# Kernel tuning notes

Measured on AMD Instinct MI355X. Metric: run time of the kernel, lower is better.

The kernel has to match this reference:

```python
import jax, jax.numpy as jnp
import numpy as np

EPS = 1e-5
HEADS, DK, DV = 8, 32, 64
SCALE = DK ** -0.5

def _bn(x, gamma, beta, mean, var):
    # eval-mode BatchNorm1d over channel dim of [b, c, n]
    inv = gamma / jnp.sqrt(var + EPS)
    return (x - mean[None, :, None]) * inv[None, :, None] + beta[None, :, None]

def setup_inputs() -> dict:
    key = jax.random.key(0)
    ks = jax.random.split(key, 24)
    dim, n, dim_out = 256, 1024, 256
    idk, idv = DK * HEADS, DV * HEADS
    def bn_params(k, c):
        k1, k2, k3, k4 = jax.random.split(k, 4)
        return (jax.random.normal(k1, (c,)) * 0.1 + 1.0,   # gamma
                jax.random.normal(k2, (c,)) * 0.1,          # beta
                jax.random.normal(k3, (c,)) * 0.1,          # running mean
                jax.random.uniform(k4, (c,)) * 0.5 + 0.5)   # running var > 0
    q_g, q_b, q_m, q_v = bn_params(ks[1], idk)
    k_g, k_b, k_m, k_v = bn_params(ks[2], idk)
    v_g, v_b, v_m, v_v = bn_params(ks[3], idv)
    o_g, o_b, o_m, o_v = bn_params(ks[4], dim_out)
    return {
        'x': jax.random.normal(ks[0], (8, dim, n), dtype=jnp.float32),
        'Wq': jax.random.normal(ks[5], (idk, dim)) * (dim ** -0.5),
        'Wk': jax.random.normal(ks[6], (idk, dim)) * (dim ** -0.5),
        'Wv': jax.random.normal(ks[7], (idv, dim)) * (dim ** -0.5),
        'Wo': jax.random.normal(ks[8], (dim_out, idv)) * (idv ** -0.5),
        'bo': jax.random.normal(ks[9], (dim_out,)) * 0.02,
        'pos_emb': jax.random.normal(ks[10], (n, HEADS)) * 0.02,
        'q_gamma': q_g, 'q_beta': q_b, 'q_mean': q_m, 'q_var': q_v,
        'k_gamma': k_g, 'k_beta': k_b, 'k_mean': k_m, 'k_var': k_v,
        'v_gamma': v_g, 'v_beta': v_b, 'v_mean': v_m, 'v_var': v_v,
        'o_gamma': o_g, 'o_beta': o_b, 'o_mean': o_m, 'o_var': o_v,
    }

def reference(x, Wq, Wk, Wv, Wo, bo, pos_emb,
              q_gamma, q_beta, q_mean, q_var,
              k_gamma, k_beta, k_mean, k_var,
              v_gamma, v_beta, v_mean, v_var,
              o_gamma, o_beta, o_mean, o_var):
    b, _, n = x.shape
    # 1x1 conv == channel matmul, then BN
    q = _bn(jnp.einsum('bcn,oc->bon', x, Wq), q_gamma, q_beta, q_mean, q_var)
    k = _bn(jnp.einsum('bcn,oc->bon', x, Wk), k_gamma, k_beta, k_mean, k_var)
    v = _bn(jnp.einsum('bcn,oc->bon', x, Wv), v_gamma, v_beta, v_mean, v_var)
    # b (h d) n -> b h n d
    q = q.reshape(b, HEADS, DK, n).transpose(0, 1, 3, 2)
    k = k.reshape(b, HEADS, DK, n).transpose(0, 1, 3, 2)
    v = v.reshape(b, HEADS, DV, n).transpose(0, 1, 3, 2)
    dots = jnp.einsum('bhid,bhjd->bhij', q, k) * SCALE
    # relative-position bias: emb[|i-j|] -> [n, n, h] -> [1, h, n, n]
    rel = jnp.abs(jnp.arange(n)[:, None] - jnp.arange(n)[None, :])
    bias = pos_emb[rel].transpose(2, 0, 1)[None]
    dots = dots + bias / SCALE
    attn = jax.nn.softmax(dots, axis=-1)
    out = jnp.einsum('bhij,bhjd->bhid', attn, v)
    # b h n d -> b (h d) n
    out = out.transpose(0, 1, 3, 2).reshape(b, HEADS * DV, n)
    out = jax.nn.gelu(out, approximate=False)
    out = jnp.einsum('bcn,oc->bon', out, Wo) + bo[None, :, None]
    return _bn(out, o_gamma, o_beta, o_mean, o_var)
```

## Files before the change

### kernel.cpp

```cpp
#include <hip/hip_runtime.h>
#include <hip/hip_bf16.h>

#define HEADS 8
#define DK 32
#define DV 64
#define DIM 256
#define NCTX 1024
#define NB 8
#define IDK 256
#define IDV 512
#define SCALE 0.17677669529663687f
#define INV_SCALE 5.656854249492381f
#define LOG2E 1.4426950408889634f
#define BN_EPS 1e-5f
#define THR 11.5416f

typedef __bf16 bf16x8 __attribute__((ext_vector_type(8)));
typedef __bf16 bf16x4 __attribute__((ext_vector_type(4)));
typedef float f32x4 __attribute__((ext_vector_type(4)));
typedef float f32x16 __attribute__((ext_vector_type(16)));

static __device__ __forceinline__ unsigned short bfbits(float v) {
  __bf16 b = (__bf16)v;
  return __builtin_bit_cast(unsigned short, b);
}

__global__ __launch_bounds__(256) void k_prep_trans(
    const float* __restrict__ x,
    const float* __restrict__ Wq, const float* __restrict__ Wk,
    const float* __restrict__ Wv, const float* __restrict__ Wo,
    const float* __restrict__ bo, const float* __restrict__ pe,
    const float* __restrict__ qg, const float* __restrict__ qb,
    const float* __restrict__ qm, const float* __restrict__ qv,
    const float* __restrict__ kg, const float* __restrict__ kb,
    const float* __restrict__ km, const float* __restrict__ kv,
    const float* __restrict__ vg, const float* __restrict__ vb,
    const float* __restrict__ vm, const float* __restrict__ vv,
    const float* __restrict__ og, const float* __restrict__ ob,
    const float* __restrict__ om, const float* __restrict__ ov,
    __bf16* __restrict__ xT, __bf16* __restrict__ WB, float* __restrict__ BB,
    uint2* __restrict__ Tq4g) {
  int bid = blockIdx.x;
  if (bid < 1605) {
    int idx = bid * 256 + threadIdx.x;
    if (idx < 65536) {
      int o = idx >> 8;
      WB[idx] = (__bf16)(Wq[idx] * (qg[o] * rsqrtf(qv[o] + BN_EPS) * SCALE * LOG2E));
    } else if (idx < 131072) {
      int i = idx - 65536, o = i >> 8;
      WB[idx] = (__bf16)(Wk[i] * (kg[o] * rsqrtf(kv[o] + BN_EPS)));
    } else if (idx < 262144) {
      int i = idx - 131072, o = i >> 8;
      WB[idx] = (__bf16)(Wv[i] * (vg[o] * rsqrtf(vv[o] + BN_EPS)));
    } else if (idx < 393216) {
      int i = idx - 262144, o = i >> 9;
      WB[idx] = (__bf16)(Wo[i] * (og[o] * rsqrtf(ov[o] + BN_EPS)));
    } else if (idx < 394496) {
      int i = idx - 393216;
      if (i < 256) {
        float sc = qg[i] * rsqrtf(qv[i] + BN_EPS);
        BB[i] = (qb[i] - qm[i] * sc) * SCALE * LOG2E;
      } else if (i < 512) {
        int o = i - 256;
        float sc = kg[o] * rsqrtf(kv[o] + BN_EPS);
        BB[i] = kb[o] - km[o] * sc;
      } else if (i < 1024) {
        int o = i - 512;
        float sc = vg[o] * rsqrtf(vv[o] + BN_EPS);
        BB[i] = vb[o] - vm[o] * sc;
      } else {
        int o = i - 1024;
        float sc = og[o] * rsqrtf(ov[o] + BN_EPS);
        BB[i] = (bo[o] - om[o]) * sc + ob[o];
      }
    } else {
      int i = idx - 394496;
      int h = i >> 11, t = i & 2047;
      unsigned short us[4];
#pragma unroll
      for (int rr = 0; rr < 4; ++rr) {
        int d = t - rr - 1023; d = d < 0 ? -d : d; d = d > 1023 ? 1023 : d;
        us[rr] = bfbits(pe[(size_t)d * HEADS + h] * INV_SCALE * LOG2E);
      }
      uint2 e;
      e.x = (unsigned)us[0] | ((unsigned)us[1] << 16);
      e.y = (unsigned)us[2] | ((unsigned)us[3] << 16);
      Tq4g[((size_t)h << 11) + t] = e;
    }
  } else {
    __shared__ float t[64][65];
    int tb = bid - 1605;
    int b = tb >> 6, c0 = ((tb >> 4) & 3) * 64, n0 = (tb & 15) * 64;
    int col = threadIdx.x & 63, rb = threadIdx.x >> 6;
    const float* xp = x + ((size_t)b * DIM + c0) * NCTX + n0;
#pragma unroll
    for (int r = 0; r < 16; ++r) {
      int row = rb + 4 * r;
      t[row][col] = xp[(size_t)row * NCTX + col];
    }
    __syncthreads();
    __bf16* op = xT + ((size_t)b * NCTX + n0) * DIM + c0;
#pragma unroll
    for (int r = 0; r < 16; ++r) {
      int i = rb + 4 * r;
      op[(size_t)i * DIM + col] = (__bf16)t[col][i];
    }
  }
}

__global__ __launch_bounds__(256, 2) void k_gemm_qkv(
    const __bf16* __restrict__ Xsrc, const __bf16* __restrict__ Wsrc,
    const float* __restrict__ Bias, __bf16* __restrict__ Qws,
    __bf16* __restrict__ Kws, __bf16* __restrict__ Vws) {
  int bx = blockIdx.x, by = blockIdx.y;
  int mode = by < 2 ? 0 : (by < 4 ? 1 : 2);
  int tid = threadIdx.x, wave = tid >> 6, lane = tid & 63;
  int wm = wave >> 1, wn = wave & 1;
  int l16 = lane & 15, g = (lane >> 4) & 3, g4 = g * 4;
  int R0 = bx * 128;

  __shared__ __align__(16) char XTl[16384];
  __shared__ __align__(16) char WTl[16384];

  int sr = tid >> 1, sh = tid & 1;
  const __bf16* xg = Xsrc + (size_t)(R0 + sr) * DIM + sh * 32;
  const __bf16* wg = Wsrc + (size_t)(by * 128 + sr) * DIM + sh * 32;
  int wbase = sr * 128;
  int gsw[4];
#pragma unroll
  for (int q = 0; q < 4; ++q) gsw[q] = ((sh * 4 + q) ^ (sr & 7)) * 16;

  bf16x8 sx[4], sw[4];
#pragma unroll
  for (int q = 0; q < 4; ++q) {
    sx[q] = *reinterpret_cast<const bf16x8*>(xg + q * 8);
    sw[q] = *reinterpret_cast<const bf16x8*>(wg + q * 8);
  }

  f32x4 acc[4][4] = {};
  const char* Abase = (mode <= 1) ? WTl : XTl;
  const char* Bbase = (mode <= 1) ? XTl : WTl;

  for (int st = 0; st < 4; ++st) {
    __syncthreads();
#pragma unroll
    for (int q = 0; q < 4; ++q) {
      *reinterpret_cast<bf16x8*>(XTl + wbase + gsw[q]) = sx[q];
      *reinterpret_cast<bf16x8*>(WTl + wbase + gsw[q]) = sw[q];
    }
    __syncthreads();
    if (st + 1 < 4) {
      const __bf16* xn = xg + (st + 1) * 64;
      const __bf16* wn_ = wg + (st + 1) * 64;
#pragma unroll
      for (int q = 0; q < 4; ++q) {
        sx[q] = *reinterpret_cast<const bf16x8*>(xn + q * 8);
        sw[q] = *reinterpret_cast<const bf16x8*>(wn_ + q * 8);
      }
    }
#pragma unroll
    for (int kc = 0; kc < 2; ++kc) {
      bf16x8 af[4], bf[4];
#pragma unroll
      for (int t = 0; t < 4; ++t) {
        int ra = wm * 64 + t * 16 + l16;
        af[t] = *reinterpret_cast<const bf16x8*>(
            Abase + ra * 128 + (((kc * 4 + g) ^ (ra & 7)) * 16));
        int rb = wn * 64 + t * 16 + l16;
        bf[t] = *reinterpret_cast<const bf16x8*>(
            Bbase + rb * 128 + (((kc * 4 + g) ^ (rb & 7)) * 16));
      }
      __builtin_amdgcn_s_setprio(1);
#pragma unroll
      for (int mt = 0; mt < 4; ++mt)
#pragma unroll
        for (int nt = 0; nt < 4; ++nt)
          acc[mt][nt] = __builtin_amdgcn_mfma_f32_16x16x32_bf16(
              af[mt], bf[nt], acc[mt][nt], 0, 0, 0);
      __builtin_amdgcn_s_setprio(0);
    }
  }

  if (mode <= 1) {
    __bf16* OWS = (mode == 0) ? Qws : Kws;
    const float* bb = Bias + (mode == 0 ? 0 : 256);
    int oq0 = by * 128 - (mode == 1 ? 256 : 0) + wm * 64;
#pragma unroll
    for (int mt = 0; mt < 4; ++mt) {
      int oq = oq0 + mt * 16 + g4;
      float4 b4 = *reinterpret_cast<const float4*>(&bb[oq]);
      int h = oq >> 5, d0 = oq & 31;
#pragma unroll
      for (int nt = 0; nt < 4; ++nt) {
        int i = R0 + wn * 64 + nt * 16 + l16;
        int b = i >> 10, n = i & 1023;
        bf16x4 pk;
        pk[0] = (__bf16)(acc[mt][nt][0] + b4.x);
        pk[1] = (__bf16)(acc[mt][nt][1] + b4.y);
        pk[2] = (__bf16)(acc[mt][nt][2] + b4.z);
        pk[3] = (__bf16)(acc[mt][nt][3] + b4.w);
        *reinterpret_cast<bf16x4*>(
            &OWS[(((size_t)b * HEADS + h) * NCTX + n) * DK + d0]) = pk;
      }
    }
  } else {
#pragma unroll
    for (int nt = 0; nt < 4; ++nt) {
      int vo = (by - 4) * 128 + wn * 64 + nt * 16 + l16;
      float bia = Bias[512 + vo];
#pragma unroll
      for (int mt = 0; mt < 4; ++mt) {
        int i0 = R0 + wm * 64 + mt * 16 + g4;
        int b = i0 >> 10, n = i0 & 1023;
        bf16x4 pk;
#pragma unroll
        for (int rr = 0; rr < 4; ++rr) pk[rr] = (__bf16)(acc[mt][nt][rr] + bia);
        *reinterpret_cast<bf16x4*>(&Vws[((size_t)b * IDV + vo) * NCTX + n]) = pk;
      }
    }
  }
}

__global__ __launch_bounds__(256, 2) void k_gemm_out(
    const __bf16* __restrict__ G, const __bf16* __restrict__ WoB,
    const float* __restrict__ bo2, float* __restrict__ out) {
  int bx = blockIdx.x, by = blockIdx.y;
  int tid = threadIdx.x, wave = tid >> 6, lane = tid & 63;
  int wm = wave >> 1, wn = wave & 1;
  int l16 = lane & 15, g = (lane >> 4) & 3, g4 = g * 4;
  int R0 = bx * 128;

  __shared__ __align__(16) char XTl[16384];
  __shared__ __align__(16) char WTl[8192];

  int sr = tid >> 1, sh = tid & 1;
  const __bf16* xg = G + (size_t)(R0 + sr) * IDV + sh * 32;
  int xbase = sr * 128;
  int gsw[4];
#pragma unroll
  for (int q = 0; q < 4; ++q) gsw[q] = ((sh * 4 + q) ^ (sr & 7)) * 16;

  int wsr = tid >> 2, wq = tid & 3;
  const __bf16* wg = WoB + (size_t)(by * 64 + wsr) * IDV + wq * 16;
  int wbase = wsr * 128;
  int gswW[2];
#pragma unroll
  for (int q = 0; q < 2; ++q) gswW[q] = ((wq * 2 + q) ^ (wsr & 7)) * 16;

  bf16x8 sx[4], sw[2];
#pragma unroll
  for (int q = 0; q < 4; ++q) sx[q] = *reinterpret_cast<const bf16x8*>(xg + q * 8);
#pragma unroll
  for (int q = 0; q < 2; ++q) sw[q] = *reinterpret_cast<const bf16x8*>(wg + q * 8);

  f32x4 acc[4][2] = {};

  for (int st = 0; st < 8; ++st) {
    __syncthreads();
#pragma unroll
    for (int q = 0; q < 4; ++q) *reinterpret_cast<bf16x8*>(XTl + xbase + gsw[q]) = sx[q];
#pragma unroll
    for (int q = 0; q < 2; ++q) *reinterpret_cast<bf16x8*>(WTl + wbase + gswW[q]) = sw[q];
    __syncthreads();
    if (st + 1 < 8) {
      const __bf16* xn = xg + (st + 1) * 64;
      const __bf16* wn_ = wg + (st + 1) * 64;
#pragma unroll
      for (int q = 0; q < 4; ++q) sx[q] = *reinterpret_cast<const bf16x8*>(xn + q * 8);
#pragma unroll
      for (int q = 0; q < 2; ++q) sw[q] = *reinterpret_cast<const bf16x8*>(wn_ + q * 8);
    }
#pragma unroll
    for (int kc = 0; kc < 2; ++kc) {
      bf16x8 af[4], bf[2];
#pragma unroll
      for (int t = 0; t < 4; ++t) {
        int ra = wm * 64 + t * 16 + l16;
        af[t] = *reinterpret_cast<const bf16x8*>(
            XTl + ra * 128 + (((kc * 4 + g) ^ (ra & 7)) * 16));
      }
#pragma unroll
      for (int t = 0; t < 2; ++t) {
        int rb = wn * 32 + t * 16 + l16;
        bf[t] = *reinterpret_cast<const bf16x8*>(
            WTl + rb * 128 + (((kc * 4 + g) ^ (rb & 7)) * 16));
      }
      __builtin_amdgcn_s_setprio(1);
#pragma unroll
      for (int mt = 0; mt < 4; ++mt)
#pragma unroll
        for (int nt = 0; nt < 2; ++nt)
          acc[mt][nt] = __builtin_amdgcn_mfma_f32_16x16x32_bf16(
              af[mt], bf[nt], acc[mt][nt], 0, 0, 0);
      __builtin_amdgcn_s_setprio(0);
    }
  }
#pragma unroll
  for (int nt = 0; nt < 2; ++nt) {
    int o = by * 64 + wn * 32 + nt * 16 + l16;
    float bia = bo2[o];
#pragma unroll
    for (int mt = 0; mt < 4; ++mt) {
      int i0 = R0 + wm * 64 + mt * 16 + g4;
      int b = i0 >> 10, n = i0 & 1023;
      float4 st;
      st.x = acc[mt][nt][0] + bia;
      st.y = acc[mt][nt][1] + bia;
      st.z = acc[mt][nt][2] + bia;
      st.w = acc[mt][nt][3] + bia;
      *reinterpret_cast<float4*>(&out[((size_t)b * DIM + o) * NCTX + n]) = st;
    }
  }
}

__global__ __launch_bounds__(128, 2) void k_attn(
    const __bf16* __restrict__ Qws, const __bf16* __restrict__ Kws,
    const __bf16* __restrict__ Vws, const uint2* __restrict__ Tq4g,
    __bf16* __restrict__ G) {
  int flat = blockIdx.x;
  int swz = (flat & 7) * 128 + (flat >> 3);
  int iblk = swz & 15, bh = swz >> 4;
  int b = bh >> 3, h = bh & 7;
  int tid = threadIdx.x, wave = tid >> 6, lane = tid & 63;
  int l31 = lane & 31, hi = lane >> 5;

  __shared__ __align__(16) __bf16 Vlds[2][64 * 64];
  __shared__ __align__(16) uint2 TqL[1088];

  int i0b = iblk * 64;
  {
    const uint4* tg4 = reinterpret_cast<const uint4*>(Tq4g + ((size_t)h << 11) + i0b);
    uint4* tl4 = reinterpret_cast<uint4*>(TqL);
    for (int c = tid; c < 544; c += 128) tl4[c] = tg4[c];
  }

  int i0w = i0b + wave * 32;
  int irow = i0w + l31;
  const __bf16* qbase = Qws + (size_t)bh * NCTX * DK;
  const __bf16* kbase = Kws + (size_t)bh * NCTX * DK;
  const __bf16* vbase = Vws + ((size_t)b * IDV + h * DV) * NCTX;
  bf16x8 qf0 = *reinterpret_cast<const bf16x8*>(qbase + (size_t)irow * DK + 8 * hi);
  bf16x8 qf1 = *reinterpret_cast<const bf16x8*>(qbase + (size_t)irow * DK + 16 + 8 * hi);

  const __bf16* kp = kbase + (size_t)l31 * DK + 8 * hi;
  bf16x8 ck0 = *reinterpret_cast<const bf16x8*>(kp);
  bf16x8 ck1 = *reinterpret_cast<const bf16x8*>(kp + 16);
  bf16x8 ck2 = *reinterpret_cast<const bf16x8*>(kp + 32 * DK);
  bf16x8 ck3 = *reinterpret_cast<const bf16x8*>(kp + 32 * DK + 16);

  int r_ = tid >> 1, vh = tid & 1;
  const __bf16* vgp = vbase + (size_t)r_ * NCTX + 8 * (vh * 4);
  int vwo[4];
#pragma unroll
  for (int q = 0; q < 4; ++q) vwo[q] = r_ * 64 + 8 * ((vh * 4 + q) ^ (r_ & 7));

  bf16x8 rv[4];
#pragma unroll
  for (int q = 0; q < 4; ++q) rv[q] = *reinterpret_cast<const bf16x8*>(vgp + q * 8);
#pragma unroll
  for (int q = 0; q < 4; ++q) *reinterpret_cast<bf16x8*>(&Vlds[0][0] + vwo[q]) = rv[q];

  f32x16 acc0 = {}, acc1 = {};
  float m = -1e30f, s = 0.0f;
  int kxb = wave * 32 + l31 + 1023 - 4 * hi;
  const bf16x4* Tqp = reinterpret_cast<const bf16x4*>(TqL);

  __syncthreads();

  for (int it = 0; it < 16; ++it) {
    int cur = it & 1, nxt = cur ^ 1;
    int j0 = it * 64;
    int jn = (j0 + 64) & (NCTX - 1);
    bf16x8 nk0 = *reinterpret_cast<const bf16x8*>(kp + (size_t)jn * DK);
    bf16x8 nk1 = *reinterpret_cast<const bf16x8*>(kp + (size_t)jn * DK + 16);
    bf16x8 nk2 = *reinterpret_cast<const bf16x8*>(kp + (size_t)(jn + 32) * DK);
    bf16x8 nk3 = *reinterpret_cast<const bf16x8*>(kp + (size_t)(jn + 32) * DK + 16);
#pragma unroll
    for (int q = 0; q < 4; ++q) rv[q] = *reinterpret_cast<const bf16x8*>(vgp + jn + q * 8);

    float sv[32];
#pragma unroll
    for (int jg = 0; jg < 2; ++jg) {
      f32x16 S = {};
      __builtin_amdgcn_s_setprio(1);
      S = __builtin_amdgcn_mfma_f32_32x32x16_bf16(jg ? ck2 : ck0, qf0, S, 0, 0, 0);
      S = __builtin_amdgcn_mfma_f32_32x32x16_bf16(jg ? ck3 : ck1, qf1, S, 0, 0, 0);
      __builtin_amdgcn_s_setprio(0);
      int kb_ = kxb - j0 - 32 * jg;
#pragma unroll
      for (int q = 0; q < 4; ++q) {
        bf16x4 q4 = Tqp[kb_ - 8 * q];
#pragma unroll
        for (int rr = 0; rr < 4; ++rr)
          sv[jg * 16 + q * 4 + rr] = S[q * 4 + rr] + (float)q4[rr];
      }
    }
    float pmax = sv[0];
#pragma unroll
    for (int k = 1; k < 32; ++k) pmax = fmaxf(pmax, sv[k]);
    if (__any(pmax > m + THR)) {
      float mx = fmaxf(pmax, __shfl_xor(pmax, 32));
      float mnew = fmaxf(m, mx);
      float corr = __builtin_amdgcn_exp2f(m - mnew);
      s *= corr; m = mnew;
#pragma unroll
      for (int r = 0; r < 16; ++r) {
        float cv = __shfl(corr, (r & 3) + 8 * (r >> 2) + 4 * hi);
        acc0[r] *= cv; acc1[r] *= cv;
      }
    }
#pragma unroll
    for (int k = 0; k < 32; ++k) sv[k] = __builtin_amdgcn_exp2f(sv[k] - m);
    float ps = 0.0f;
#pragma unroll
    for (int k = 0; k < 32; ++k) ps += sv[k];
    s += ps;
#pragma unroll
    for (int jg = 0; jg < 2; ++jg) {
#pragma unroll
      for (int u = 0; u < 2; ++u) {
        int base = jg * 16 + 8 * u;
        unsigned we0, we1, wo0, wo1;
        asm("v_cvt_pk_bf16_f32 %0, %1, %2" : "=v"(we0) : "v"(sv[base + 0]), "v"(sv[base + 1]));
        asm("v_cvt_pk_bf16_f32 %0, %1, %2" : "=v"(we1) : "v"(sv[base + 2]), "v"(sv[base + 3]));
        asm("v_cvt_pk_bf16_f32 %0, %1, %2" : "=v"(wo0) : "v"(sv[base + 4]), "v"(sv[base + 5]));
        asm("v_cvt_pk_bf16_f32 %0, %1, %2" : "=v"(wo1) : "v"(sv[base + 6]), "v"(sv[base + 7]));
        asm volatile("v_permlane32_swap_b32 %0, %1" : "+v"(we0), "+v"(wo0));
        asm volatile("v_permlane32_swap_b32 %0, %1" : "+v"(we1), "+v"(wo1));
        uint4 pw = {we0, we1, wo0, wo1};
        bf16x8 pfrag = *reinterpret_cast<bf16x8*>(&pw);
        int sl = 2 * (jg * 2 + u) + hi;
        bf16x8 vf0 = *reinterpret_cast<const bf16x8*>(
            &Vlds[cur][0] + l31 * 64 + 8 * (sl ^ (l31 & 7)));
        bf16x8 vf1 = *reinterpret_cast<const bf16x8*>(
            &Vlds[cur][0] + (32 + l31) * 64 + 8 * (sl ^ (l31 & 7)));
        __builtin_amdgcn_s_setprio(1);
        acc0 = __builtin_amdgcn_mfma_f32_32x32x16_bf16(pfrag, vf0, acc0, 0, 0, 0);
        acc1 = __builtin_amdgcn_mfma_f32_32x32x16_bf16(pfrag, vf1, acc1, 0, 0, 0);
        __builtin_amdgcn_s_setprio(0);
      }
    }
    ck0 = nk0; ck1 = nk1; ck2 = nk2; ck3 = nk3;
#pragma unroll
    for (int q = 0; q < 4; ++q) *reinterpret_cast<bf16x8*>(&Vlds[nxt][0] + vwo[q]) = rv[q];
    __syncthreads();
  }
  float srow = s + __shfl_xor(s, 32);
  float inv = 1.0f / srow;
  __bf16* gbase = G + (size_t)b * NCTX * IDV + h * DV + l31;
#pragma unroll
  for (int r = 0; r < 16; ++r) {
    int il = (r & 3) + 8 * (r >> 2) + 4 * hi;
    float iv = __shfl(inv, il);
    float v0 = acc0[r] * iv, v1 = acc1[r] * iv;
    float g0 = 0.5f * v0 * (1.0f + erff(v0 * 0.70710678118654752f));
    float g1 = 0.5f * v1 * (1.0f + erff(v1 * 0.70710678118654752f));
    gbase[(size_t)(i0w + il) * IDV] = (__bf16)g0;
    gbase[(size_t)(i0w + il) * IDV + 32] = (__bf16)g1;
  }
}

extern "C" void kernel_launch(void* const* d_in, const int* in_sizes, int n_in,
                              void* d_out, int out_size, void* d_ws, size_t ws_size,
                              hipStream_t stream) {
  const float* x  = (const float*)d_in[0];
  const float* Wq = (const float*)d_in[1];
  const float* Wk = (const float*)d_in[2];
  const float* Wv = (const float*)d_in[3];
  const float* Wo = (const float*)d_in[4];
  const float* bo = (const float*)d_in[5];
  const float* pe = (const float*)d_in[6];
  const float* qg = (const float*)d_in[7];
  const float* qb = (const float*)d_in[8];
  const float* qm = (const float*)d_in[9];
  const float* qv = (const float*)d_in[10];
  const float* kg = (const float*)d_in[11];
  const float* kb = (const float*)d_in[12];
  const float* km = (const float*)d_in[13];
  const float* kv = (const float*)d_in[14];
  const float* vg = (const float*)d_in[15];
  const float* vb = (const float*)d_in[16];
  const float* vm = (const float*)d_in[17];
  const float* vv = (const float*)d_in[18];
  const float* og = (const float*)d_in[19];
  const float* ob = (const float*)d_in[20];
  const float* om = (const float*)d_in[21];
  const float* ov = (const float*)d_in[22];

  char* ws = (char*)d_ws;
  __bf16* xT = (__bf16*)(ws);
  __bf16* Q  = (__bf16*)(ws + (4ull << 20));
  __bf16* K  = (__bf16*)(ws + (8ull << 20));
  __bf16* V  = (__bf16*)(ws + (12ull << 20));
  __bf16* G  = (__bf16*)(ws + (20ull << 20));
  __bf16* WB = (__bf16*)(ws + (28ull << 20));
  float*  BB = (float*)(ws + (28ull << 20) + (768ull << 10));
  uint2*  Tq = (uint2*)(ws + (29ull << 20));
  float* out = (float*)d_out;

  k_prep_trans<<<dim3(2117), 256, 0, stream>>>(
      x, Wq, Wk, Wv, Wo, bo, pe, qg, qb, qm, qv, kg, kb, km, kv,
      vg, vb, vm, vv, og, ob, om, ov, xT, WB, BB, Tq);
  k_gemm_qkv<<<dim3(64, 8), 256, 0, stream>>>(xT, WB, BB, Q, K, V);
  k_attn<<<dim3(1024), 128, 0, stream>>>(Q, K, V, Tq, G);
  k_gemm_out<<<dim3(64, 4), 256, 0, stream>>>(G, WB + 262144, BB + 1024, out);
}
```

Baseline: 59.48 us.

## Split attention over key halves with a separate combine kernel

```diff
diff --git a/kernel.cpp b/kernel.cpp
--- a/kernel.cpp
+++ b/kernel.cpp
@@ -313,27 +313,24 @@
   }
 }
 
-__global__ __launch_bounds__(128, 2) void k_attn(
+__global__ __launch_bounds__(128, 3) void k_attn(
     const __bf16* __restrict__ Qws, const __bf16* __restrict__ Kws,
     const __bf16* __restrict__ Vws, const uint2* __restrict__ Tq4g,
-    __bf16* __restrict__ G) {
+    __bf16* __restrict__ Opart, float* __restrict__ MS) {
   int flat = blockIdx.x;
-  int swz = (flat & 7) * 128 + (flat >> 3);
+  int jh = flat >> 10;
+  int rest = flat & 1023;
+  int swz = (rest & 7) * 128 + (rest >> 3);
   int iblk = swz & 15, bh = swz >> 4;
   int b = bh >> 3, h = bh & 7;
   int tid = threadIdx.x, wave = tid >> 6, lane = tid & 63;
   int l31 = lane & 31, hi = lane >> 5;
-
+  int jbase = jh * 512;
+
+  __shared__ __align__(16) __bf16 Klds[2][64][40];
   __shared__ __align__(16) __bf16 Vlds[2][64 * 64];
-  __shared__ __align__(16) uint2 TqL[1088];
 
   int i0b = iblk * 64;
-  {
-    const uint4* tg4 = reinterpret_cast<const uint4*>(Tq4g + ((size_t)h << 11) + i0b);
-    uint4* tl4 = reinterpret_cast<uint4*>(TqL);
-    for (int c = tid; c < 544; c += 128) tl4[c] = tg4[c];
-  }
-
   int i0w = i0b + wave * 32;
   int irow = i0w + l31;
   const __bf16* qbase = Qws + (size_t)bh * NCTX * DK;
@@ -342,54 +339,55 @@
   bf16x8 qf0 = *reinterpret_cast<const bf16x8*>(qbase + (size_t)irow * DK + 8 * hi);
   bf16x8 qf1 = *reinterpret_cast<const bf16x8*>(qbase + (size_t)irow * DK + 16 + 8 * hi);
 
-  const __bf16* kp = kbase + (size_t)l31 * DK + 8 * hi;
-  bf16x8 ck0 = *reinterpret_cast<const bf16x8*>(kp);
-  bf16x8 ck1 = *reinterpret_cast<const bf16x8*>(kp + 16);
-  bf16x8 ck2 = *reinterpret_cast<const bf16x8*>(kp + 32 * DK);
-  bf16x8 ck3 = *reinterpret_cast<const bf16x8*>(kp + 32 * DK + 16);
-
+  int rk_ = tid >> 1, sk2 = tid & 1;
+  const __bf16* kgp = kbase + (size_t)(jbase + rk_) * DK + 16 * sk2;
+  int ko0 = rk_ * 40 + 16 * sk2, ko1 = ko0 + 8;
   int r_ = tid >> 1, vh = tid & 1;
-  const __bf16* vgp = vbase + (size_t)r_ * NCTX + 8 * (vh * 4);
+  const __bf16* vgp = vbase + (size_t)r_ * NCTX + jbase + 8 * (vh * 4);
   int vwo[4];
 #pragma unroll
   for (int q = 0; q < 4; ++q) vwo[q] = r_ * 64 + 8 * ((vh * 4 + q) ^ (r_ & 7));
 
+  bf16x8 rk0 = *reinterpret_cast<const bf16x8*>(kgp);
+  bf16x8 rk1 = *reinterpret_cast<const bf16x8*>(kgp + 8);
   bf16x8 rv[4];
 #pragma unroll
   for (int q = 0; q < 4; ++q) rv[q] = *reinterpret_cast<const bf16x8*>(vgp + q * 8);
+  *reinterpret_cast<bf16x8*>(&Klds[0][0][0] + ko0) = rk0;
+  *reinterpret_cast<bf16x8*>(&Klds[0][0][0] + ko1) = rk1;
 #pragma unroll
   for (int q = 0; q < 4; ++q) *reinterpret_cast<bf16x8*>(&Vlds[0][0] + vwo[q]) = rv[q];
 
   f32x16 acc0 = {}, acc1 = {};
   float m = -1e30f, s = 0.0f;
-  int kxb = wave * 32 + l31 + 1023 - 4 * hi;
-  const bf16x4* Tqp = reinterpret_cast<const bf16x4*>(TqL);
+  int kxg = irow + 1023 - 4 * hi;
+  const bf16x4* TqG = reinterpret_cast<const bf16x4*>(Tq4g + ((size_t)h << 11));
 
   __syncthreads();
 
-  for (int it = 0; it < 16; ++it) {
+  for (int it = 0; it < 8; ++it) {
     int cur = it & 1, nxt = cur ^ 1;
-    int j0 = it * 64;
-    int jn = (j0 + 64) & (NCTX - 1);
-    bf16x8 nk0 = *reinterpret_cast<const bf16x8*>(kp + (size_t)jn * DK);
-    bf16x8 nk1 = *reinterpret_cast<const bf16x8*>(kp + (size_t)jn * DK + 16);
-    bf16x8 nk2 = *reinterpret_cast<const bf16x8*>(kp + (size_t)(jn + 32) * DK);
-    bf16x8 nk3 = *reinterpret_cast<const bf16x8*>(kp + (size_t)(jn + 32) * DK + 16);
+    int j0 = jbase + it * 64;
+    int jn = ((it + 1) & 7) * 64;
+    rk0 = *reinterpret_cast<const bf16x8*>(kgp + (size_t)jn * DK);
+    rk1 = *reinterpret_cast<const bf16x8*>(kgp + (size_t)jn * DK + 8);
 #pragma unroll
     for (int q = 0; q < 4; ++q) rv[q] = *reinterpret_cast<const bf16x8*>(vgp + jn + q * 8);
 
     float sv[32];
 #pragma unroll
     for (int jg = 0; jg < 2; ++jg) {
+      bf16x8 kf0 = *reinterpret_cast<const bf16x8*>(&Klds[cur][32 * jg + l31][8 * hi]);
+      bf16x8 kf1 = *reinterpret_cast<const bf16x8*>(&Klds[cur][32 * jg + l31][16 + 8 * hi]);
       f32x16 S = {};
       __builtin_amdgcn_s_setprio(1);
-      S = __builtin_amdgcn_mfma_f32_32x32x16_bf16(jg ? ck2 : ck0, qf0, S, 0, 0, 0);
-      S = __builtin_amdgcn_mfma_f32_32x32x16_bf16(jg ? ck3 : ck1, qf1, S, 0, 0, 0);
+      S = __builtin_amdgcn_mfma_f32_32x32x16_bf16(kf0, qf0, S, 0, 0, 0);
+      S = __builtin_amdgcn_mfma_f32_32x32x16_bf16(kf1, qf1, S, 0, 0, 0);
       __builtin_amdgcn_s_setprio(0);
-      int kb_ = kxb - j0 - 32 * jg;
+      int kb_ = kxg - j0 - 32 * jg;
 #pragma unroll
       for (int q = 0; q < 4; ++q) {
-        bf16x4 q4 = Tqp[kb_ - 8 * q];
+        bf16x4 q4 = TqG[kb_ - 8 * q];
 #pragma unroll
         for (int rr = 0; rr < 4; ++rr)
           sv[jg * 16 + q * 4 + rr] = S[q * 4 + rr] + (float)q4[rr];
@@ -440,23 +438,59 @@
         __builtin_amdgcn_s_setprio(0);
       }
     }
-    ck0 = nk0; ck1 = nk1; ck2 = nk2; ck3 = nk3;
+    *reinterpret_cast<bf16x8*>(&Klds[nxt][0][0] + ko0) = rk0;
+    *reinterpret_cast<bf16x8*>(&Klds[nxt][0][0] + ko1) = rk1;
 #pragma unroll
     for (int q = 0; q < 4; ++q) *reinterpret_cast<bf16x8*>(&Vlds[nxt][0] + vwo[q]) = rv[q];
     __syncthreads();
   }
   float srow = s + __shfl_xor(s, 32);
-  float inv = 1.0f / srow;
-  __bf16* gbase = G + (size_t)b * NCTX * IDV + h * DV + l31;
+  int blk = bh * 16 + iblk;
+  __bf16* Op = Opart + ((size_t)(jh * 1024 + blk)) * 4096;
+  float* MSp = MS + ((size_t)(jh * 1024 + blk)) * 128;
+  if (hi == 0) {
+    MSp[wave * 32 + l31] = m;
+    MSp[64 + wave * 32 + l31] = srow;
+  }
 #pragma unroll
   for (int r = 0; r < 16; ++r) {
-    int il = (r & 3) + 8 * (r >> 2) + 4 * hi;
-    float iv = __shfl(inv, il);
-    float v0 = acc0[r] * iv, v1 = acc1[r] * iv;
-    float g0 = 0.5f * v0 * (1.0f + erff(v0 * 0.70710678118654752f));
-    float g1 = 0.5f * v1 * (1.0f + erff(v1 * 0.70710678118654752f));
-    gbase[(size_t)(i0w + il) * IDV] = (__bf16)g0;
-    gbase[(size_t)(i0w + il) * IDV + 32] = (__bf16)g1;
+    int row = wave * 32 + (r & 3) + 8 * (r >> 2) + 4 * hi;
+    Op[row * 64 + l31] = (__bf16)acc0[r];
+    Op[row * 64 + 32 + l31] = (__bf16)acc1[r];
+  }
+}
+
+__global__ __launch_bounds__(128) void k_comb(
+    const __bf16* __restrict__ Opart, const float* __restrict__ MS,
+    __bf16* __restrict__ G) {
+  int blk = blockIdx.x;
+  int bh = blk >> 4, iblk = blk & 15;
+  int b = bh >> 3, h = bh & 7;
+  int tid = threadIdx.x;
+  int row = tid >> 1, dh = tid & 1;
+  const __bf16* O1 = Opart + (size_t)blk * 4096 + row * 64 + dh * 32;
+  const __bf16* O2 = Opart + (size_t)(1024 + blk) * 4096 + row * 64 + dh * 32;
+  const float* M1 = MS + (size_t)blk * 128;
+  const float* M2 = MS + (size_t)(1024 + blk) * 128;
+  float m1 = M1[row], s1 = M1[64 + row];
+  float m2 = M2[row], s2 = M2[64 + row];
+  float M = fmaxf(m1, m2);
+  float w1 = __builtin_amdgcn_exp2f(m1 - M);
+  float w2 = __builtin_amdgcn_exp2f(m2 - M);
+  float inv = 1.0f / (s1 * w1 + s2 * w2);
+  w1 *= inv; w2 *= inv;
+  __bf16* gp = G + (size_t)b * NCTX * IDV + (size_t)(iblk * 64 + row) * IDV + h * DV + dh * 32;
+#pragma unroll
+  for (int q = 0; q < 4; ++q) {
+    bf16x8 o1 = *reinterpret_cast<const bf16x8*>(O1 + q * 8);
+    bf16x8 o2 = *reinterpret_cast<const bf16x8*>(O2 + q * 8);
+    bf16x8 rg;
+#pragma unroll
+    for (int j = 0; j < 8; ++j) {
+      float v = (float)o1[j] * w1 + (float)o2[j] * w2;
+      rg[j] = (__bf16)(0.5f * v * (1.0f + erff(v * 0.70710678118654752f)));
+    }
+    *reinterpret_cast<bf16x8*>(gp + q * 8) = rg;
   }
 }
 
@@ -496,12 +530,15 @@
   __bf16* WB = (__bf16*)(ws + (28ull << 20));
   float*  BB = (float*)(ws + (28ull << 20) + (768ull << 10));
   uint2*  Tq = (uint2*)(ws + (29ull << 20));
+  __bf16* Op = (__bf16*)(ws + (32ull << 20));
+  float*  MSb = (float*)(ws + (52ull << 20));
   float* out = (float*)d_out;
 
   k_prep_trans<<<dim3(2117), 256, 0, stream>>>(
       x, Wq, Wk, Wv, Wo, bo, pe, qg, qb, qm, qv, kg, kb, km, kv,
       vg, vb, vm, vv, og, ob, om, ov, xT, WB, BB, Tq);
   k_gemm_qkv<<<dim3(64, 8), 256, 0, stream>>>(xT, WB, BB, Q, K, V);
-  k_attn<<<dim3(1024), 128, 0, stream>>>(Q, K, V, Tq, G);
+  k_attn<<<dim3(2048), 128, 0, stream>>>(Q, K, V, Tq, Op, MSb);
+  k_comb<<<dim3(1024), 128, 0, stream>>>(Op, MSb, G);
   k_gemm_out<<<dim3(64, 4), 256, 0, stream>>>(G, WB + 262144, BB + 1024, out);
 }
```

Result: slower. 74.59 us (+25.4%).

## Process two query tiles per wave and stage K through shared memory

Applied to the files above, without the earlier changes.

```diff
diff --git a/kernel.cpp b/kernel.cpp
--- a/kernel.cpp
+++ b/kernel.cpp
@@ -318,51 +318,54 @@
     const __bf16* __restrict__ Vws, const uint2* __restrict__ Tq4g,
     __bf16* __restrict__ G) {
   int flat = blockIdx.x;
-  int swz = (flat & 7) * 128 + (flat >> 3);
-  int iblk = swz & 15, bh = swz >> 4;
+  int swz = (flat & 7) * 64 + (flat >> 3);
+  int iblk = swz & 7, bh = swz >> 3;
   int b = bh >> 3, h = bh & 7;
   int tid = threadIdx.x, wave = tid >> 6, lane = tid & 63;
   int l31 = lane & 31, hi = lane >> 5;
 
+  __shared__ __align__(16) __bf16 Klds[2][64][40];
   __shared__ __align__(16) __bf16 Vlds[2][64 * 64];
-  __shared__ __align__(16) uint2 TqL[1088];
-
-  int i0b = iblk * 64;
+  __shared__ __align__(16) uint2 TqL[1152];
+
+  int i0b = iblk * 128;
   {
     const uint4* tg4 = reinterpret_cast<const uint4*>(Tq4g + ((size_t)h << 11) + i0b);
     uint4* tl4 = reinterpret_cast<uint4*>(TqL);
-    for (int c = tid; c < 544; c += 128) tl4[c] = tg4[c];
-  }
-
-  int i0w = i0b + wave * 32;
-  int irow = i0w + l31;
+    for (int c = tid; c < 576; c += 128) tl4[c] = tg4[c];
+  }
+
+  int i0w = i0b + wave * 64;
   const __bf16* qbase = Qws + (size_t)bh * NCTX * DK;
   const __bf16* kbase = Kws + (size_t)bh * NCTX * DK;
   const __bf16* vbase = Vws + ((size_t)b * IDV + h * DV) * NCTX;
-  bf16x8 qf0 = *reinterpret_cast<const bf16x8*>(qbase + (size_t)irow * DK + 8 * hi);
-  bf16x8 qf1 = *reinterpret_cast<const bf16x8*>(qbase + (size_t)irow * DK + 16 + 8 * hi);
-
-  const __bf16* kp = kbase + (size_t)l31 * DK + 8 * hi;
-  bf16x8 ck0 = *reinterpret_cast<const bf16x8*>(kp);
-  bf16x8 ck1 = *reinterpret_cast<const bf16x8*>(kp + 16);
-  bf16x8 ck2 = *reinterpret_cast<const bf16x8*>(kp + 32 * DK);
-  bf16x8 ck3 = *reinterpret_cast<const bf16x8*>(kp + 32 * DK + 16);
-
-  int r_ = tid >> 1, vh = tid & 1;
-  const __bf16* vgp = vbase + (size_t)r_ * NCTX + 8 * (vh * 4);
+  bf16x8 qf00 = *reinterpret_cast<const bf16x8*>(qbase + (size_t)(i0w + l31) * DK + 8 * hi);
+  bf16x8 qf01 = *reinterpret_cast<const bf16x8*>(qbase + (size_t)(i0w + l31) * DK + 16 + 8 * hi);
+  bf16x8 qf10 = *reinterpret_cast<const bf16x8*>(qbase + (size_t)(i0w + 32 + l31) * DK + 8 * hi);
+  bf16x8 qf11 = *reinterpret_cast<const bf16x8*>(qbase + (size_t)(i0w + 32 + l31) * DK + 16 + 8 * hi);
+
+  int r_ = tid >> 1, half = tid & 1;
+  const __bf16* kgp = kbase + (size_t)r_ * DK + 16 * half;
+  int ko0 = r_ * 40 + 16 * half, ko1 = ko0 + 8;
+  const __bf16* vgp = vbase + (size_t)r_ * NCTX + 8 * (half * 4);
   int vwo[4];
 #pragma unroll
-  for (int q = 0; q < 4; ++q) vwo[q] = r_ * 64 + 8 * ((vh * 4 + q) ^ (r_ & 7));
-
+  for (int q = 0; q < 4; ++q) vwo[q] = r_ * 64 + 8 * ((half * 4 + q) ^ (r_ & 7));
+
+  bf16x8 rk0 = *reinterpret_cast<const bf16x8*>(kgp);
+  bf16x8 rk1 = *reinterpret_cast<const bf16x8*>(kgp + 8);
   bf16x8 rv[4];
 #pragma unroll
   for (int q = 0; q < 4; ++q) rv[q] = *reinterpret_cast<const bf16x8*>(vgp + q * 8);
+  *reinterpret_cast<bf16x8*>(&Klds[0][0][0] + ko0) = rk0;
+  *reinterpret_cast<bf16x8*>(&Klds[0][0][0] + ko1) = rk1;
 #pragma unroll
   for (int q = 0; q < 4; ++q) *reinterpret_cast<bf16x8*>(&Vlds[0][0] + vwo[q]) = rv[q];
 
-  f32x16 acc0 = {}, acc1 = {};
-  float m = -1e30f, s = 0.0f;
-  int kxb = wave * 32 + l31 + 1023 - 4 * hi;
+  f32x16 acc00 = {}, acc01 = {}, acc10 = {}, acc11 = {};
+  float m0 = -1e30f, s0 = 0.0f, m1 = -1e30f, s1 = 0.0f;
+  int kxb0 = wave * 64 + l31 + 1023 - 4 * hi;
+  int kxb1 = kxb0 + 32;
   const bf16x4* Tqp = reinterpret_cast<const bf16x4*>(TqL);
 
   __syncthreads();
@@ -371,92 +374,149 @@
     int cur = it & 1, nxt = cur ^ 1;
     int j0 = it * 64;
     int jn = (j0 + 64) & (NCTX - 1);
-    bf16x8 nk0 = *reinterpret_cast<const bf16x8*>(kp + (size_t)jn * DK);
-    bf16x8 nk1 = *reinterpret_cast<const bf16x8*>(kp + (size_t)jn * DK + 16);
-    bf16x8 nk2 = *reinterpret_cast<const bf16x8*>(kp + (size_t)(jn + 32) * DK);
-    bf16x8 nk3 = *reinterpret_cast<const bf16x8*>(kp + (size_t)(jn + 32) * DK + 16);
+    rk0 = *reinterpret_cast<const bf16x8*>(kgp + (size_t)jn * DK);
+    rk1 = *reinterpret_cast<const bf16x8*>(kgp + (size_t)jn * DK + 8);
 #pragma unroll
     for (int q = 0; q < 4; ++q) rv[q] = *reinterpret_cast<const bf16x8*>(vgp + jn + q * 8);
 
-    float sv[32];
+    float sv0[32], sv1[32];
 #pragma unroll
     for (int jg = 0; jg < 2; ++jg) {
-      f32x16 S = {};
+      bf16x8 kf0 = *reinterpret_cast<const bf16x8*>(&Klds[cur][32 * jg + l31][8 * hi]);
+      bf16x8 kf1 = *reinterpret_cast<const bf16x8*>(&Klds[cur][32 * jg + l31][16 + 8 * hi]);
+      f32x16 S0 = {}, S1 = {};
       __builtin_amdgcn_s_setprio(1);
-      S = __builtin_amdgcn_mfma_f32_32x32x16_bf16(jg ? ck2 : ck0, qf0, S, 0, 0, 0);
-      S = __builtin_amdgcn_mfma_f32_32x32x16_bf16(jg ? ck3 : ck1, qf1, S, 0, 0, 0);
+      S0 = __builtin_amdgcn_mfma_f32_32x32x16_bf16(kf0, qf00, S0, 0, 0, 0);
+      S1 = __builtin_amdgcn_mfma_f32_32x32x16_bf16(kf0, qf10, S1, 0, 0, 0);
+      S0 = __builtin_amdgcn_mfma_f32_32x32x16_bf16(kf1, qf01, S0, 0, 0, 0);
+      S1 = __builtin_amdgcn_mfma_f32_32x32x16_bf16(kf1, qf11, S1, 0, 0, 0);
       __builtin_amdgcn_s_setprio(0);
-      int kb_ = kxb - j0 - 32 * jg;
+      int kb0 = kxb0 - j0 - 32 * jg;
+      int kb1 = kxb1 - j0 - 32 * jg;
 #pragma unroll
       for (int q = 0; q < 4; ++q) {
-        bf16x4 q4 = Tqp[kb_ - 8 * q];
-#pragma unroll
-        for (int rr = 0; rr < 4; ++rr)
-          sv[jg * 16 + q * 4 + rr] = S[q * 4 + rr] + (float)q4[rr];
-      }
-    }
-    float pmax = sv[0];
-#pragma unroll
-    for (int k = 1; k < 32; ++k) pmax = fmaxf(pmax, sv[k]);
-    if (__any(pmax > m + THR)) {
-      float mx = fmaxf(pmax, __shfl_xor(pmax, 32));
-      float mnew = fmaxf(m, mx);
-      float corr = __builtin_amdgcn_exp2f(m - mnew);
-      s *= corr; m = mnew;
-#pragma unroll
-      for (int r = 0; r < 16; ++r) {
-        float cv = __shfl(corr, (r & 3) + 8 * (r >> 2) + 4 * hi);
-        acc0[r] *= cv; acc1[r] *= cv;
-      }
-    }
-#pragma unroll
-    for (int k = 0; k < 32; ++k) sv[k] = __builtin_amdgcn_exp2f(sv[k] - m);
-    float ps = 0.0f;
-#pragma unroll
-    for (int k = 0; k < 32; ++k) ps += sv[k];
-    s += ps;
+        bf16x4 q40 = Tqp[kb0 - 8 * q];
+        bf16x4 q41 = Tqp[kb1 - 8 * q];
+#pragma unroll
+        for (int rr = 0; rr < 4; ++rr) {
+          sv0[jg * 16 + q * 4 + rr] = S0[q * 4 + rr] + (float)q40[rr];
+          sv1[jg * 16 + q * 4 + rr] = S1[q * 4 + rr] + (float)q41[rr];
+        }
+      }
+    }
+    {
+      float pmax = sv0[0];
+#pragma unroll
+      for (int k = 1; k < 32; ++k) pmax = fmaxf(pmax, sv0[k]);
+      if (__any(pmax > m0 + THR)) {
+        float mx = fmaxf(pmax, __shfl_xor(pmax, 32));
+        float mnew = fmaxf(m0, mx);
+        float corr = __builtin_amdgcn_exp2f(m0 - mnew);
+        s0 *= corr; m0 = mnew;
+#pragma unroll
+        for (int r = 0; r < 16; ++r) {
+          float cv = __shfl(corr, (r & 3) + 8 * (r >> 2) + 4 * hi);
+          acc00[r] *= cv; acc01[r] *= cv;
+        }
+      }
+#pragma unroll
+      for (int k = 0; k < 32; ++k) sv0[k] = __builtin_amdgcn_exp2f(sv0[k] - m0);
+      float ps = 0.0f;
+#pragma unroll
+      for (int k = 0; k < 32; ++k) ps += sv0[k];
+      s0 += ps;
+    }
+    {
+      float pmax = sv1[0];
+#pragma unroll
+      for (int k = 1; k < 32; ++k) pmax = fmaxf(pmax, sv1[k]);
+      if (__any(pmax > m1 + THR)) {
+        float mx = fmaxf(pmax, __shfl_xor(pmax, 32));
+        float mnew = fmaxf(m1, mx);
+        float corr = __builtin_amdgcn_exp2f(m1 - mnew);
+        s1 *= corr; m1 = mnew;
+#pragma unroll
+        for (int r = 0; r < 16; ++r) {
+          float cv = __shfl(corr, (r & 3) + 8 * (r >> 2) + 4 * hi);
+          acc10[r] *= cv; acc11[r] *= cv;
+        }
+      }
+#pragma unroll
+      for (int k = 0; k < 32; ++k) sv1[k] = __builtin_amdgcn_exp2f(sv1[k] - m1);
+      float ps = 0.0f;
+#pragma unroll
+      for (int k = 0; k < 32; ++k) ps += sv1[k];
+      s1 += ps;
+    }
 #pragma unroll
     for (int jg = 0; jg < 2; ++jg) {
 #pragma unroll
       for (int u = 0; u < 2; ++u) {
         int base = jg * 16 + 8 * u;
-        unsigned we0, we1, wo0, wo1;
-        asm("v_cvt_pk_bf16_f32 %0, %1, %2" : "=v"(we0) : "v"(sv[base + 0]), "v"(sv[base + 1]));
-        asm("v_cvt_pk_bf16_f32 %0, %1, %2" : "=v"(we1) : "v"(sv[base + 2]), "v"(sv[base + 3]));
-        asm("v_cvt_pk_bf16_f32 %0, %1, %2" : "=v"(wo0) : "v"(sv[base + 4]), "v"(sv[base + 5]));
-        asm("v_cvt_pk_bf16_f32 %0, %1, %2" : "=v"(wo1) : "v"(sv[base + 6]), "v"(sv[base + 7]));
-        asm volatile("v_permlane32_swap_b32 %0, %1" : "+v"(we0), "+v"(wo0));
-        asm volatile("v_permlane32_swap_b32 %0, %1" : "+v"(we1), "+v"(wo1));
-        uint4 pw = {we0, we1, wo0, wo1};
-        bf16x8 pfrag = *reinterpret_cast<bf16x8*>(&pw);
+        unsigned a0, a1, b0, b1, c0, c1, d0, d1;
+        asm("v_cvt_pk_bf16_f32 %0, %1, %2" : "=v"(a0) : "v"(sv0[base + 0]), "v"(sv0[base + 1]));
+        asm("v_cvt_pk_bf16_f32 %0, %1, %2" : "=v"(a1) : "v"(sv0[base + 2]), "v"(sv0[base + 3]));
+        asm("v_cvt_pk_bf16_f32 %0, %1, %2" : "=v"(b0) : "v"(sv0[base + 4]), "v"(sv0[base + 5]));
+        asm("v_cvt_pk_bf16_f32 %0, %1, %2" : "=v"(b1) : "v"(sv0[base + 6]), "v"(sv0[base + 7]));
+        asm volatile("v_permlane32_swap_b32 %0, %1" : "+v"(a0), "+v"(b0));
+        asm volatile("v_permlane32_swap_b32 %0, %1" : "+v"(a1), "+v"(b1));
+        asm("v_cvt_pk_bf16_f32 %0, %1, %2" : "=v"(c0) : "v"(sv1[base + 0]), "v"(sv1[base + 1]));
+        asm("v_cvt_pk_bf16_f32 %0, %1, %2" : "=v"(c1) : "v"(sv1[base + 2]), "v"(sv1[base + 3]));
+        asm("v_cvt_pk_bf16_f32 %0, %1, %2" : "=v"(d0) : "v"(sv1[base + 4]), "v"(sv1[base + 5]));
+        asm("v_cvt_pk_bf16_f32 %0, %1, %2" : "=v"(d1) : "v"(sv1[base + 6]), "v"(sv1[base + 7]));
+        asm volatile("v_permlane32_swap_b32 %0, %1" : "+v"(c0), "+v"(d0));
+        asm volatile("v_permlane32_swap_b32 %0, %1" : "+v"(c1), "+v"(d1));
+        uint4 pw0 = {a0, a1, b0, b1};
+        uint4 pw1 = {c0, c1, d0, d1};
+        bf16x8 pf0 = *reinterpret_cast<bf16x8*>(&pw0);
+        bf16x8 pf1 = *reinterpret_cast<bf16x8*>(&pw1);
         int sl = 2 * (jg * 2 + u) + hi;
         bf16x8 vf0 = *reinterpret_cast<const bf16x8*>(
             &Vlds[cur][0] + l31 * 64 + 8 * (sl ^ (l31 & 7)));
         bf16x8 vf1 = *reinterpret_cast<const bf16x8*>(
             &Vlds[cur][0] + (32 + l31) * 64 + 8 * (sl ^ (l31 & 7)));
         __builtin_amdgcn_s_setprio(1);
-        acc0 = __builtin_amdgcn_mfma_f32_32x32x16_bf16(pfrag, vf0, acc0, 0, 0, 0);
-        acc1 = __builtin_amdgcn_mfma_f32_32x32x16_bf16(pfrag, vf1, acc1, 0, 0, 0);
+        acc00 = __builtin_amdgcn_mfma_f32_32x32x16_bf16(pf0, vf0, acc00, 0, 0, 0);
+        acc01 = __builtin_amdgcn_mfma_f32_32x32x16_bf16(pf0, vf1, acc01, 0, 0, 0);
+        acc10 = __builtin_amdgcn_mfma_f32_32x32x16_bf16(pf1, vf0, acc10, 0, 0, 0);
+        acc11 = __builtin_amdgcn_mfma_f32_32x32x16_bf16(pf1, vf1, acc11, 0, 0, 0);
         __builtin_amdgcn_s_setprio(0);
       }
     }
-    ck0 = nk0; ck1 = nk1; ck2 = nk2; ck3 = nk3;
+    *reinterpret_cast<bf16x8*>(&Klds[nxt][0][0] + ko0) = rk0;
+    *reinterpret_cast<bf16x8*>(&Klds[nxt][0][0] + ko1) = rk1;
 #pragma unroll
     for (int q = 0; q < 4; ++q) *reinterpret_cast<bf16x8*>(&Vlds[nxt][0] + vwo[q]) = rv[q];
     __syncthreads();
   }
-  float srow = s + __shfl_xor(s, 32);
-  float inv = 1.0f / srow;
   __bf16* gbase = G + (size_t)b * NCTX * IDV + h * DV + l31;
-#pragma unroll
-  for (int r = 0; r < 16; ++r) {
-    int il = (r & 3) + 8 * (r >> 2) + 4 * hi;
-    float iv = __shfl(inv, il);
-    float v0 = acc0[r] * iv, v1 = acc1[r] * iv;
-    float g0 = 0.5f * v0 * (1.0f + erff(v0 * 0.70710678118654752f));
-    float g1 = 0.5f * v1 * (1.0f + erff(v1 * 0.70710678118654752f));
-    gbase[(size_t)(i0w + il) * IDV] = (__bf16)g0;
-    gbase[(size_t)(i0w + il) * IDV + 32] = (__bf16)g1;
+  {
+    float srow = s0 + __shfl_xor(s0, 32);
+    float inv = 1.0f / srow;
+#pragma unroll
+    for (int r = 0; r < 16; ++r) {
+      int il = (r & 3) + 8 * (r >> 2) + 4 * hi;
+      float iv = __shfl(inv, il);
+      float v0 = acc00[r] * iv, v1 = acc01[r] * iv;
+      float g0 = 0.5f * v0 * (1.0f + erff(v0 * 0.70710678118654752f));
+      float g1 = 0.5f * v1 * (1.0f + erff(v1 * 0.70710678118654752f));
+      gbase[(size_t)(i0w + il) * IDV] = (__bf16)g0;
+      gbase[(size_t)(i0w + il) * IDV + 32] = (__bf16)g1;
+    }
+  }
+  {
+    float srow = s1 + __shfl_xor(s1, 32);
+    float inv = 1.0f / srow;
+#pragma unroll
+    for (int r = 0; r < 16; ++r) {
+      int il = (r & 3) + 8 * (r >> 2) + 4 * hi;
+      float iv = __shfl(inv, il);
+      float v0 = acc10[r] * iv, v1 = acc11[r] * iv;
+      float g0 = 0.5f * v0 * (1.0f + erff(v0 * 0.70710678118654752f));
+      float g1 = 0.5f * v1 * (1.0f + erff(v1 * 0.70710678118654752f));
+      gbase[(size_t)(i0w + 32 + il) * IDV] = (__bf16)g0;
+      gbase[(size_t)(i0w + 32 + il) * IDV + 32] = (__bf16)g1;
+    }
   }
 }
 
@@ -502,6 +562,6 @@
       x, Wq, Wk, Wv, Wo, bo, pe, qg, qb, qm, qv, kg, kb, km, kv,
       vg, vb, vm, vv, og, ob, om, ov, xT, WB, BB, Tq);
   k_gemm_qkv<<<dim3(64, 8), 256, 0, stream>>>(xT, WB, BB, Q, K, V);
-  k_attn<<<dim3(1024), 128, 0, stream>>>(Q, K, V, Tq, G);
+  k_attn<<<dim3(512), 128, 0, stream>>>(Q, K, V, Tq, G);
   k_gemm_out<<<dim3(64, 4), 256, 0, stream>>>(G, WB + 262144, BB + 1024, out);
 }
```

After: 78.67 us. 32.3% more time.
